# Kernel optimization log

Hardware: AMD Instinct MI355X
Metric: run time of the kernel (lower is better)

## Reference

```python
import jax, jax.numpy as jnp
import numpy as np

NUM_USERS = 100000
NUM_ITEMS = 50000
EMBED_DIM = 64
N_LAYERS = 3
NUM_EDGES = 3276800  # avg user degree 32
BATCH = 16384


def setup_inputs() -> dict:
    key = jax.random.key(0)
    k0, k1, k2, k3, k4, k5 = jax.random.split(key, 6)
    rows = jax.random.randint(k0, (NUM_EDGES,), 0, NUM_USERS, dtype=jnp.int32)
    cols = jax.random.randint(k1, (NUM_EDGES,), 0, NUM_ITEMS, dtype=jnp.int32)
    user_table = jax.random.normal(k2, (NUM_USERS, EMBED_DIM), dtype=jnp.float32) * 0.1
    item_table = jax.random.normal(k3, (NUM_ITEMS, EMBED_DIM), dtype=jnp.float32) * 0.1
    user_indices = jax.random.randint(k4, (BATCH,), 0, NUM_USERS, dtype=jnp.int32)
    item_indices = jax.random.randint(k5, (BATCH,), 0, NUM_ITEMS, dtype=jnp.int32)
    return {
        "user_table": user_table,
        "item_table": item_table,
        "rows": rows,
        "cols": cols,
        "user_indices": user_indices,
        "item_indices": item_indices,
    }


def reference(user_table, item_table, rows, cols, user_indices, item_indices):
    # D^-1 A row-normalization of the binary bipartite adjacency:
    # normalized edge value for edge (u, i) is 1 / deg(u) (0 if isolated).
    ones = jnp.ones(rows.shape, dtype=user_table.dtype)
    deg = jax.ops.segment_sum(ones, rows, num_segments=NUM_USERS)
    inv_deg = jnp.where(deg > 0, 1.0 / deg, 0.0)
    vals = inv_deg[rows]  # [E]

    u = user_table  # [U, D] (unused by propagation in the original too)
    it = item_table  # [I, D]
    for _ in range(N_LAYERS):
        # u = A @ it  (SpMM via gather + segment-sum over destination users)
        u = jax.ops.segment_sum(vals[:, None] * it[cols], rows, num_segments=NUM_USERS)
        # it = A^T @ u
        it = jax.ops.segment_sum(vals[:, None] * u[rows], cols, num_segments=NUM_ITEMS)

    scores = jnp.sum(u[user_indices] * it[item_indices], axis=-1)  # [B]
    return jax.nn.sigmoid(scores)
```

## Files before the change

kernel.cpp:

```cpp
#include <hip/hip_runtime.h>
#include <math.h>

#define NUM_USERS 100000
#define NUM_ITEMS 50000
#define EMBED     64
#define NUM_EDGES 3276800
#define BATCH     16384
#define CAP       10752
#define NBUCK     391
#define P1_EDGES  16384
#define P1_THREADS 512

typedef _Float16 half8 __attribute__((ext_vector_type(8)));

__global__ void cvt_kernel(const float* __restrict__ in, _Float16* __restrict__ out, int n8) {
    int i = blockIdx.x * 256 + threadIdx.x;
    if (i >= n8) return;
    const float4* p = (const float4*)in + 2 * i;
    float4 a = p[0], b = p[1];
    half8 o;
    o[0] = (_Float16)a.x; o[1] = (_Float16)a.y; o[2] = (_Float16)a.z; o[3] = (_Float16)a.w;
    o[4] = (_Float16)b.x; o[5] = (_Float16)b.y; o[6] = (_Float16)b.z; o[7] = (_Float16)b.w;
    ((half8*)out)[i] = o;
}

__global__ void __launch_bounds__(P1_THREADS)
pass1_kernel(const int* __restrict__ rows, const int* __restrict__ cols,
             int* __restrict__ ucur, int* __restrict__ icur,
             int* __restrict__ rec_u, int* __restrict__ rec_i) {
    __shared__ int hu[400], hi[400], gu[400], gi[400];
    __shared__ int lbase[400], lcur[400];
    __shared__ int sc[512];
    __shared__ int recbuf[P1_EDGES];
    int t = threadIdx.x;
    for (int i = t; i < 400; i += P1_THREADS) { hu[i] = 0; hi[i] = 0; }
    __syncthreads();
    long long e0 = (long long)blockIdx.x * P1_EDGES;
    for (int i = t; i < P1_EDGES; i += P1_THREADS) {
        atomicAdd(&hu[rows[e0 + i] >> 8], 1);
        atomicAdd(&hi[cols[e0 + i] >> 7], 1);
    }
    __syncthreads();
    for (int i = t; i < 400; i += P1_THREADS) {
        int vr = (hu[i] + 15) & ~15;
        gu[i] = vr ? atomicAdd(&ucur[i], vr) : 0;
        vr = (hi[i] + 15) & ~15;
        gi[i] = vr ? atomicAdd(&icur[i], vr) : 0;
    }

    __syncthreads();
    sc[t] = (t < 400) ? hu[t] : 0;
    __syncthreads();
    for (int o = 1; o < 512; o <<= 1) {
        int x = (t >= o) ? sc[t - o] : 0; __syncthreads();
        sc[t] += x; __syncthreads();
    }
    if (t < 400) { lbase[t] = sc[t] - hu[t]; lcur[t] = 0; }
    __syncthreads();
    for (int i = t; i < P1_EDGES; i += P1_THREADS) {
        int r = rows[e0 + i], c = cols[e0 + i];
        int b = r >> 8;
        int p = lbase[b] + atomicAdd(&lcur[b], 1);
        recbuf[p] = (c << 8) | (r & 255);
    }
    __syncthreads();
    sc[t] = (t < 400) ? ((hu[t] + 15) & ~15) : 0;
    __syncthreads();
    for (int o = 1; o < 512; o <<= 1) {
        int x = (t >= o) ? sc[t - o] : 0; __syncthreads();
        sc[t] += x; __syncthreads();
    }
    int total = sc[511];
    for (int o4 = t * 4; o4 < total; o4 += P1_THREADS * 4) {
        int lo = 0, hi_ = 399;
        while (lo < hi_) { int mid = (lo + hi_) >> 1; if (sc[mid] > o4) hi_ = mid; else lo = mid + 1; }
        int b = lo;
        int v = hu[b];
        int vr = (v + 15) & ~15;
        int j = o4 - (sc[b] - vr);
        int gpos = gu[b] + j;
        if (gpos + 3 < CAP) {
            int4 val;
            val.x = (j + 0 < v) ? recbuf[lbase[b] + j + 0] : -1;
            val.y = (j + 1 < v) ? recbuf[lbase[b] + j + 1] : -1;
            val.z = (j + 2 < v) ? recbuf[lbase[b] + j + 2] : -1;
            val.w = (j + 3 < v) ? recbuf[lbase[b] + j + 3] : -1;
            *(int4*)(rec_u + (long long)b * CAP + gpos) = val;
        } else {
            for (int k = 0; k < 4; ++k)
                if (gpos + k < CAP)
                    rec_u[(long long)b * CAP + gpos + k] = (j + k < v) ? recbuf[lbase[b] + j + k] : -1;
        }
    }

    __syncthreads();
    sc[t] = (t < 400) ? hi[t] : 0;
    __syncthreads();
    for (int o = 1; o < 512; o <<= 1) {
        int x = (t >= o) ? sc[t - o] : 0; __syncthreads();
        sc[t] += x; __syncthreads();
    }
    if (t < 400) { lbase[t] = sc[t] - hi[t]; lcur[t] = 0; }
    __syncthreads();
    for (int i = t; i < P1_EDGES; i += P1_THREADS) {
        int r = rows[e0 + i], c = cols[e0 + i];
        int b = c >> 7;
        int p = lbase[b] + atomicAdd(&lcur[b], 1);
        recbuf[p] = (r << 7) | (c & 127);
    }
    __syncthreads();
    sc[t] = (t < 400) ? ((hi[t] + 15) & ~15) : 0;
    __syncthreads();
    for (int o = 1; o < 512; o <<= 1) {
        int x = (t >= o) ? sc[t - o] : 0; __syncthreads();
        sc[t] += x; __syncthreads();
    }
    total = sc[511];
    for (int o4 = t * 4; o4 < total; o4 += P1_THREADS * 4) {
        int lo = 0, hi_ = 399;
        while (lo < hi_) { int mid = (lo + hi_) >> 1; if (sc[mid] > o4) hi_ = mid; else lo = mid + 1; }
        int b = lo;
        int v = hi[b];
        int vr = (v + 15) & ~15;
        int j = o4 - (sc[b] - vr);
        int gpos = gi[b] + j;
        if (gpos + 3 < CAP) {
            int4 val;
            val.x = (j + 0 < v) ? recbuf[lbase[b] + j + 0] : -1;
            val.y = (j + 1 < v) ? recbuf[lbase[b] + j + 1] : -1;
            val.z = (j + 2 < v) ? recbuf[lbase[b] + j + 2] : -1;
            val.w = (j + 3 < v) ? recbuf[lbase[b] + j + 3] : -1;
            *(int4*)(rec_i + (long long)b * CAP + gpos) = val;
        } else {
            for (int k = 0; k < 4; ++k)
                if (gpos + k < CAP)
                    rec_i[(long long)b * CAP + gpos + k] = (j + k < v) ? recbuf[lbase[b] + j + k] : -1;
        }
    }
}

template <int VBITS>
__global__ void pass2_kernel(int* __restrict__ rec, const int* __restrict__ cur,
                             int* __restrict__ deg, int* __restrict__ off,
                             float* __restrict__ inv32, int ncap) {
    const int V = 1 << VBITS, M = V - 1;
    __shared__ int buf[CAP];
    __shared__ int h[256], ex[256], cnt[256], sc[256];
    int t = threadIdx.x, b = blockIdx.x;
    long long s = (long long)b * CAP;
    int n = cur[b]; if (n > CAP) n = CAP;
    for (int i = t; i < n; i += 256) buf[i] = rec[s + i];
    if (t < V) { h[t] = 0; cnt[t] = 0; }
    __syncthreads();
    for (int i = t; i < n; i += 256) {
        int r = buf[i];
        if (r != -1) atomicAdd(&h[r & M], 1);
    }
    __syncthreads();
    if (t < V) sc[t] = h[t];
    __syncthreads();
    for (int o = 1; o < V; o <<= 1) {
        int x = (t >= o && t < V) ? sc[t - o] : 0;
        __syncthreads();
        if (t < V) sc[t] += x;
        __syncthreads();
    }
    if (t < V) {
        ex[t] = sc[t] - h[t];
        int id = b * V + t;
        if (id < ncap) {
            int v = h[t];
            deg[id] = v;
            off[id] = (int)(s + ex[t]);
            if (inv32) inv32[id] = v ? 1.0f / (float)v : 0.0f;
        }
    }
    __syncthreads();
    for (int i = t; i < n; i += 256) {
        int r = buf[i];
        if (r == -1) continue;
        int k = r & M;
        int rnk = atomicAdd(&cnt[k], 1);
        rec[s + ex[k] + rnk] = (int)(((unsigned)r) >> VBITS);
    }
}

__global__ void mark_kernel(const int* __restrict__ iidx, unsigned char* __restrict__ bm) {
    int i = blockIdx.x * 256 + threadIdx.x;
    if (i < BATCH) bm[iidx[i]] = 1;
}

__global__ void compact_kernel(const unsigned char* __restrict__ bm,
                               int* __restrict__ list, int* __restrict__ cnt) {
    int i = blockIdx.x * 256 + threadIdx.x;
    if (i < NUM_ITEMS && bm[i]) {
        int p = atomicAdd(cnt, 1);
        list[p] = i;
    }
}

__global__ void gather_u(const int* __restrict__ uoff, const int* __restrict__ udeg,
                         const int* __restrict__ csr_col, const float* __restrict__ inv32,
                         const _Float16* __restrict__ it, _Float16* __restrict__ w) {
    int row = blockIdx.x * 4 + (threadIdx.x >> 6);
    if (row >= NUM_USERS) return;
    int lane = threadIdx.x & 63;
    int slot = lane >> 3;
    int h    = lane & 7;
    int start = uoff[row];
    int end = start + udeg[row];
    half8 acc = {0, 0, 0, 0, 0, 0, 0, 0};
    for (int k = start; k < end; k += 32) {
        int e1 = end - 1;
        int i0 = k + slot, i1 = i0 + 8, i2 = i0 + 16, i3 = i0 + 24;
        int c0 = csr_col[i0 < e1 ? i0 : e1];
        int c1 = csr_col[i1 < e1 ? i1 : e1];
        int c2 = csr_col[i2 < e1 ? i2 : e1];
        int c3 = csr_col[i3 < e1 ? i3 : e1];
        c0 = i0 < end ? c0 : NUM_ITEMS;
        c1 = i1 < end ? c1 : NUM_ITEMS;
        c2 = i2 < end ? c2 : NUM_ITEMS;
        c3 = i3 < end ? c3 : NUM_ITEMS;
        half8 x0 = *(const half8*)(it + (long long)c0 * EMBED + (h << 3));
        half8 x1 = *(const half8*)(it + (long long)c1 * EMBED + (h << 3));
        half8 x2 = *(const half8*)(it + (long long)c2 * EMBED + (h << 3));
        half8 x3 = *(const half8*)(it + (long long)c3 * EMBED + (h << 3));
        acc += x0; acc += x1; acc += x2; acc += x3;
    }
    float f[8];
    #pragma unroll
    for (int j = 0; j < 8; ++j) {
        f[j] = (float)acc[j];
        f[j] += __shfl_xor(f[j], 8, 64);
        f[j] += __shfl_xor(f[j], 16, 64);
        f[j] += __shfl_xor(f[j], 32, 64);
    }
    if (lane < 8) {
        float v = inv32[row];
        float v2 = v * v;
        half8 ow;
        #pragma unroll
        for (int j = 0; j < 8; ++j) ow[j] = (_Float16)(f[j] * v2);
        *(half8*)(w + (long long)row * EMBED + (lane << 3)) = ow;
    }
}

__device__ __forceinline__ void gather_it_body(int col, int lane,
                                               const int* __restrict__ ioff,
                                               const int* __restrict__ ideg,
                                               const int* __restrict__ csc_row,
                                               const _Float16* __restrict__ w,
                                               _Float16* __restrict__ it) {
    int slot = lane >> 3;
    int h    = lane & 7;
    int start = ioff[col];
    int end = start + ideg[col];
    half8 acc = {0, 0, 0, 0, 0, 0, 0, 0};
    for (int k = start; k < end; k += 64) {
        int e1 = end - 1;
        int idx[8], r[8];
        #pragma unroll
        for (int q = 0; q < 8; ++q) {
            idx[q] = k + slot + q * 8;
            int safe = idx[q] < e1 ? idx[q] : e1;
            r[q] = csc_row[safe];
            r[q] = idx[q] < end ? r[q] : NUM_USERS;
        }
        half8 x[8];
        #pragma unroll
        for (int q = 0; q < 8; ++q)
            x[q] = *(const half8*)(w + (long long)r[q] * EMBED + (h << 3));
        #pragma unroll
        for (int q = 0; q < 8; ++q) acc += x[q];
    }
    float f[8];
    #pragma unroll
    for (int j = 0; j < 8; ++j) {
        f[j] = (float)acc[j];
        f[j] += __shfl_xor(f[j], 8, 64);
        f[j] += __shfl_xor(f[j], 16, 64);
        f[j] += __shfl_xor(f[j], 32, 64);
    }
    if (lane < 8) {
        half8 o;
        #pragma unroll
        for (int j = 0; j < 8; ++j) o[j] = (_Float16)f[j];
        *(half8*)(it + (long long)col * EMBED + (lane << 3)) = o;
    }
}

__global__ void gather_it(const int* __restrict__ ioff, const int* __restrict__ ideg,
                          const int* __restrict__ csc_row,
                          const _Float16* __restrict__ w, _Float16* __restrict__ it) {
    int col = blockIdx.x * 4 + (threadIdx.x >> 6);
    if (col >= NUM_ITEMS) return;
    gather_it_body(col, threadIdx.x & 63, ioff, ideg, csc_row, w, it);
}

__global__ void gather_it_list(const int* __restrict__ ioff, const int* __restrict__ ideg,
                               const int* __restrict__ csc_row,
                               const _Float16* __restrict__ w, _Float16* __restrict__ it,
                               const int* __restrict__ list, const int* __restrict__ cnt) {
    int idx = blockIdx.x * 4 + (threadIdx.x >> 6);
    if (idx >= *cnt) return;
    gather_it_body(list[idx], threadIdx.x & 63, ioff, ideg, csc_row, w, it);
}

__global__ void score_kernel(const _Float16* __restrict__ w, const _Float16* __restrict__ it,
                             const int* __restrict__ udeg,
                             const int* __restrict__ uidx, const int* __restrict__ iidx,
                             float* __restrict__ out) {
    int wave_in_block = threadIdx.x >> 6;
    int lane = threadIdx.x & 63;
    int b = blockIdx.x * 4 + wave_in_block;
    if (b >= BATCH) return;
    int ui = uidx[b];
    int ii = iidx[b];
    float s = (float)w[(long long)ui * EMBED + lane] * (float)it[(long long)ii * EMBED + lane];
    #pragma unroll
    for (int off = 32; off > 0; off >>= 1)
        s += __shfl_down(s, off, 64);
    if (lane == 0) {
        s *= (float)udeg[ui];
        out[b] = 1.0f / (1.0f + expf(-s));
    }
}

extern "C" void kernel_launch(void* const* d_in, const int* in_sizes, int n_in,
                              void* d_out, int out_size, void* d_ws, size_t ws_size,
                              hipStream_t stream) {
    const float* item_table = (const float*)d_in[1];
    const int*   rows       = (const int*)d_in[2];
    const int*   cols       = (const int*)d_in[3];
    const int*   uidx       = (const int*)d_in[4];
    const int*   iidx       = (const int*)d_in[5];
    float* out = (float*)d_out;

    char* base = (char*)d_ws;
    int*   udeg  = (int*)(base + 0);
    int*   ideg  = (int*)(base +   400000);
    int*   uoff  = (int*)(base +   600000);
    int*   ioff  = (int*)(base +  1000000);
    float* inv32 = (float*)(base + 1200000);
    int*   ucur  = (int*)(base +  1600000);
    int*   icur  = (int*)(base +  1601600);
    int*   lcnt  = (int*)(base +  1603200);
    int*   ilist = (int*)(base +  1603264);
    unsigned char* bm = (unsigned char*)(base + 1668800);
    int*   rec_u = (int*)(base +  1720320);
    int*   rec_i = (int*)(base + 18923520);
    _Float16* w16  = (_Float16*)(base + 36126720);
    _Float16* it16 = (_Float16*)(base + 48926848);

    (void)hipMemsetAsync(base + 1600000, 0, 3204, stream);
    (void)hipMemsetAsync(bm, 0, NUM_ITEMS, stream);
    (void)hipMemsetAsync(w16 + (long long)NUM_USERS * EMBED, 0, 128, stream);
    (void)hipMemsetAsync(it16 + (long long)NUM_ITEMS * EMBED, 0, 128, stream);

    cvt_kernel<<<(NUM_ITEMS * EMBED / 8 + 255) / 256, 256, 0, stream>>>(
        item_table, it16, NUM_ITEMS * EMBED / 8);

    pass1_kernel<<<NUM_EDGES / P1_EDGES, P1_THREADS, 0, stream>>>(
        rows, cols, ucur, icur, rec_u, rec_i);
    pass2_kernel<8><<<NBUCK, 256, 0, stream>>>(rec_u, ucur, udeg, uoff, inv32, NUM_USERS);
    pass2_kernel<7><<<NBUCK, 256, 0, stream>>>(rec_i, icur, ideg, ioff, (float*)nullptr, NUM_ITEMS);

    mark_kernel<<<BATCH / 256, 256, 0, stream>>>(iidx, bm);
    compact_kernel<<<(NUM_ITEMS + 255) / 256, 256, 0, stream>>>(bm, ilist, lcnt);

    const int ublocks = (NUM_USERS + 3) / 4;
    const int iblocks = (NUM_ITEMS + 3) / 4;
    for (int l = 0; l < 3; ++l) {
        gather_u<<<ublocks, 256, 0, stream>>>(uoff, udeg, rec_u, inv32, it16, w16);
        if (l < 2)
            gather_it<<<iblocks, 256, 0, stream>>>(ioff, ideg, rec_i, w16, it16);
        else
            gather_it_list<<<BATCH / 4, 256, 0, stream>>>(ioff, ideg, rec_i, w16, it16,
                                                          ilist, lcnt);
    }

    score_kernel<<<BATCH / 4, 256, 0, stream>>>(w16, it16, udeg, uidx, iidx, out);
}
```

Before: 477.4 us.

## Merge setup kernels, cache edge loads in registers, drop item-list compaction

The separate memsets and the fp16 conversion become one prep kernel, and the two pass2 bucket-sort launches merge into one grid. pass1 loads each thread's 32 rows/cols into registers once instead of re-reading global memory three times. The mark/compact step that built a unique item list is removed; the final item gather now runs directly over all batch item indices, which may recompute duplicate items redundantly. The intent is fewer launches and less global traffic, at the cost of more register pressure in pass1 and some duplicate writes in the last layer.

```diff
diff --git a/kernel.cpp b/kernel.cpp
--- a/kernel.cpp
+++ b/kernel.cpp
@@ -8,20 +8,34 @@
 #define BATCH     16384
 #define CAP       10752
 #define NBUCK     391
+#define NBUCK_I   391
 #define P1_EDGES  16384
 #define P1_THREADS 512
+#define CVT_BLOCKS 1563
 
 typedef _Float16 half8 __attribute__((ext_vector_type(8)));
 
-__global__ void cvt_kernel(const float* __restrict__ in, _Float16* __restrict__ out, int n8) {
-    int i = blockIdx.x * 256 + threadIdx.x;
-    if (i >= n8) return;
-    const float4* p = (const float4*)in + 2 * i;
-    float4 a = p[0], b = p[1];
-    half8 o;
-    o[0] = (_Float16)a.x; o[1] = (_Float16)a.y; o[2] = (_Float16)a.z; o[3] = (_Float16)a.w;
-    o[4] = (_Float16)b.x; o[5] = (_Float16)b.y; o[6] = (_Float16)b.z; o[7] = (_Float16)b.w;
-    ((half8*)out)[i] = o;
+__global__ void prep_kernel(const float* __restrict__ itab, _Float16* __restrict__ it16,
+                            int* __restrict__ curzero,
+                            _Float16* __restrict__ w16) {
+    int b = blockIdx.x;
+    if (b < CVT_BLOCKS) {
+        int i = b * 256 + threadIdx.x;
+        if (i < NUM_ITEMS * EMBED / 8) {
+            const float4* p = (const float4*)itab + 2 * i;
+            float4 a = p[0], c = p[1];
+            half8 o;
+            o[0] = (_Float16)a.x; o[1] = (_Float16)a.y; o[2] = (_Float16)a.z; o[3] = (_Float16)a.w;
+            o[4] = (_Float16)c.x; o[5] = (_Float16)c.y; o[6] = (_Float16)c.z; o[7] = (_Float16)c.w;
+            ((half8*)it16)[i] = o;
+        }
+    } else if (b == CVT_BLOCKS) {
+        for (int k = threadIdx.x; k < 800; k += 256) curzero[k] = 0;
+    } else {
+        int i = threadIdx.x;
+        if (i < 64) w16[(long long)NUM_USERS * EMBED + i] = (_Float16)0.f;
+        else if (i < 128) it16[(long long)NUM_ITEMS * EMBED + (i - 64)] = (_Float16)0.f;
+    }
 }
 
 __global__ void __launch_bounds__(P1_THREADS)
@@ -33,12 +47,21 @@
     __shared__ int sc[512];
     __shared__ int recbuf[P1_EDGES];
     int t = threadIdx.x;
+    long long e0 = (long long)blockIdx.x * P1_EDGES;
+
+    int er[32], ec[32];
+    #pragma unroll
+    for (int q = 0; q < 32; ++q) {
+        er[q] = rows[e0 + t + q * P1_THREADS];
+        ec[q] = cols[e0 + t + q * P1_THREADS];
+    }
+
     for (int i = t; i < 400; i += P1_THREADS) { hu[i] = 0; hi[i] = 0; }
     __syncthreads();
-    long long e0 = (long long)blockIdx.x * P1_EDGES;
-    for (int i = t; i < P1_EDGES; i += P1_THREADS) {
-        atomicAdd(&hu[rows[e0 + i] >> 8], 1);
-        atomicAdd(&hi[cols[e0 + i] >> 7], 1);
+    #pragma unroll
+    for (int q = 0; q < 32; ++q) {
+        atomicAdd(&hu[er[q] >> 8], 1);
+        atomicAdd(&hi[ec[q] >> 7], 1);
     }
     __syncthreads();
     for (int i = t; i < 400; i += P1_THREADS) {
@@ -57,11 +80,11 @@
     }
     if (t < 400) { lbase[t] = sc[t] - hu[t]; lcur[t] = 0; }
     __syncthreads();
-    for (int i = t; i < P1_EDGES; i += P1_THREADS) {
-        int r = rows[e0 + i], c = cols[e0 + i];
-        int b = r >> 8;
+    #pragma unroll
+    for (int q = 0; q < 32; ++q) {
+        int b = er[q] >> 8;
         int p = lbase[b] + atomicAdd(&lcur[b], 1);
-        recbuf[p] = (c << 8) | (r & 255);
+        recbuf[p] = (ec[q] << 8) | (er[q] & 255);
     }
     __syncthreads();
     sc[t] = (t < 400) ? ((hu[t] + 15) & ~15) : 0;
@@ -102,11 +125,11 @@
     }
     if (t < 400) { lbase[t] = sc[t] - hi[t]; lcur[t] = 0; }
     __syncthreads();
-    for (int i = t; i < P1_EDGES; i += P1_THREADS) {
-        int r = rows[e0 + i], c = cols[e0 + i];
-        int b = c >> 7;
+    #pragma unroll
+    for (int q = 0; q < 32; ++q) {
+        int b = ec[q] >> 7;
         int p = lbase[b] + atomicAdd(&lcur[b], 1);
-        recbuf[p] = (r << 7) | (c & 127);
+        recbuf[p] = (er[q] << 7) | (ec[q] & 127);
     }
     __syncthreads();
     sc[t] = (t < 400) ? ((hi[t] + 15) & ~15) : 0;
@@ -140,13 +163,12 @@
 }
 
 template <int VBITS>
-__global__ void pass2_kernel(int* __restrict__ rec, const int* __restrict__ cur,
-                             int* __restrict__ deg, int* __restrict__ off,
-                             float* __restrict__ inv32, int ncap) {
+__device__ __forceinline__ void pass2_body(int* __restrict__ rec, const int* __restrict__ cur,
+                                           int* __restrict__ deg, int* __restrict__ off,
+                                           float* __restrict__ inv32, int ncap, int b,
+                                           int* buf, int* h, int* ex, int* cnt, int* sc) {
     const int V = 1 << VBITS, M = V - 1;
-    __shared__ int buf[CAP];
-    __shared__ int h[256], ex[256], cnt[256], sc[256];
-    int t = threadIdx.x, b = blockIdx.x;
+    int t = threadIdx.x;
     long long s = (long long)b * CAP;
     int n = cur[b]; if (n > CAP) n = CAP;
     for (int i = t; i < n; i += 256) buf[i] = rec[s + i];
@@ -185,18 +207,19 @@
     }
 }
 
-__global__ void mark_kernel(const int* __restrict__ iidx, unsigned char* __restrict__ bm) {
-    int i = blockIdx.x * 256 + threadIdx.x;
-    if (i < BATCH) bm[iidx[i]] = 1;
-}
-
-__global__ void compact_kernel(const unsigned char* __restrict__ bm,
-                               int* __restrict__ list, int* __restrict__ cnt) {
-    int i = blockIdx.x * 256 + threadIdx.x;
-    if (i < NUM_ITEMS && bm[i]) {
-        int p = atomicAdd(cnt, 1);
-        list[p] = i;
-    }
+__global__ void __launch_bounds__(256)
+pass2_kernel(int* __restrict__ rec_u, const int* __restrict__ ucur,
+             int* __restrict__ udeg, int* __restrict__ uoff, float* __restrict__ inv32,
+             int* __restrict__ rec_i, const int* __restrict__ icur,
+             int* __restrict__ ideg, int* __restrict__ ioff) {
+    __shared__ int buf[CAP];
+    __shared__ int h[256], ex[256], cnt[256], sc[256];
+    if (blockIdx.x < NBUCK)
+        pass2_body<8>(rec_u, ucur, udeg, uoff, inv32, NUM_USERS, blockIdx.x,
+                      buf, h, ex, cnt, sc);
+    else
+        pass2_body<7>(rec_i, icur, ideg, ioff, (float*)nullptr, NUM_ITEMS,
+                      blockIdx.x - NBUCK, buf, h, ex, cnt, sc);
 }
 
 __global__ void gather_u(const int* __restrict__ uoff, const int* __restrict__ udeg,
@@ -297,13 +320,13 @@
     gather_it_body(col, threadIdx.x & 63, ioff, ideg, csc_row, w, it);
 }
 
-__global__ void gather_it_list(const int* __restrict__ ioff, const int* __restrict__ ideg,
-                               const int* __restrict__ csc_row,
-                               const _Float16* __restrict__ w, _Float16* __restrict__ it,
-                               const int* __restrict__ list, const int* __restrict__ cnt) {
-    int idx = blockIdx.x * 4 + (threadIdx.x >> 6);
-    if (idx >= *cnt) return;
-    gather_it_body(list[idx], threadIdx.x & 63, ioff, ideg, csc_row, w, it);
+__global__ void gather_it_batch(const int* __restrict__ ioff, const int* __restrict__ ideg,
+                                const int* __restrict__ csc_row,
+                                const _Float16* __restrict__ w, _Float16* __restrict__ it,
+                                const int* __restrict__ iidx) {
+    int b = blockIdx.x * 4 + (threadIdx.x >> 6);
+    if (b >= BATCH) return;
+    gather_it_body(iidx[b], threadIdx.x & 63, ioff, ideg, csc_row, w, it);
 }
 
 __global__ void score_kernel(const _Float16* __restrict__ w, const _Float16* __restrict__ it,
@@ -344,29 +367,17 @@
     float* inv32 = (float*)(base + 1200000);
     int*   ucur  = (int*)(base +  1600000);
     int*   icur  = (int*)(base +  1601600);
-    int*   lcnt  = (int*)(base +  1603200);
-    int*   ilist = (int*)(base +  1603264);
-    unsigned char* bm = (unsigned char*)(base + 1668800);
     int*   rec_u = (int*)(base +  1720320);
     int*   rec_i = (int*)(base + 18923520);
     _Float16* w16  = (_Float16*)(base + 36126720);
     _Float16* it16 = (_Float16*)(base + 48926848);
 
-    (void)hipMemsetAsync(base + 1600000, 0, 3204, stream);
-    (void)hipMemsetAsync(bm, 0, NUM_ITEMS, stream);
-    (void)hipMemsetAsync(w16 + (long long)NUM_USERS * EMBED, 0, 128, stream);
-    (void)hipMemsetAsync(it16 + (long long)NUM_ITEMS * EMBED, 0, 128, stream);
-
-    cvt_kernel<<<(NUM_ITEMS * EMBED / 8 + 255) / 256, 256, 0, stream>>>(
-        item_table, it16, NUM_ITEMS * EMBED / 8);
+    prep_kernel<<<CVT_BLOCKS + 2, 256, 0, stream>>>(item_table, it16, ucur, w16);
 
     pass1_kernel<<<NUM_EDGES / P1_EDGES, P1_THREADS, 0, stream>>>(
         rows, cols, ucur, icur, rec_u, rec_i);
-    pass2_kernel<8><<<NBUCK, 256, 0, stream>>>(rec_u, ucur, udeg, uoff, inv32, NUM_USERS);
-    pass2_kernel<7><<<NBUCK, 256, 0, stream>>>(rec_i, icur, ideg, ioff, (float*)nullptr, NUM_ITEMS);
-
-    mark_kernel<<<BATCH / 256, 256, 0, stream>>>(iidx, bm);
-    compact_kernel<<<(NUM_ITEMS + 255) / 256, 256, 0, stream>>>(bm, ilist, lcnt);
+    pass2_kernel<<<NBUCK + NBUCK_I, 256, 0, stream>>>(rec_u, ucur, udeg, uoff, inv32,
+                                                      rec_i, icur, ideg, ioff);
 
     const int ublocks = (NUM_USERS + 3) / 4;
     const int iblocks = (NUM_ITEMS + 3) / 4;
@@ -375,8 +386,7 @@
         if (l < 2)
             gather_it<<<iblocks, 256, 0, stream>>>(ioff, ideg, rec_i, w16, it16);
         else
-            gather_it_list<<<BATCH / 4, 256, 0, stream>>>(ioff, ideg, rec_i, w16, it16,
-                                                          ilist, lcnt);
+            gather_it_batch<<<BATCH / 4, 256, 0, stream>>>(ioff, ideg, rec_i, w16, it16, iidx);
     }
 
     score_kernel<<<BATCH / 4, 256, 0, stream>>>(w16, it16, udeg, uidx, iidx, out);
```

Result: faster. 431.8 us (-9.6%).
